# Optimization experiments

Measured on AMD Instinct MI355X. Metric: run time of the kernel, lower is better.

Reference implementation:

```python
import jax, jax.numpy as jnp
import numpy as np

N_HEADS = 64
HEAD_DIM = 128
ROPE_DIM = 64
TOPK = 2048
ROPE_BASE = 10000.0


def _rope(x, positions):
    # neox-style rotary on the first ROPE_DIM dims of the last axis
    half = ROPE_DIM // 2
    inv_freq = 1.0 / (ROPE_BASE ** (jnp.arange(half, dtype=jnp.float32) / half))
    ang = positions.astype(jnp.float32)[:, None] * inv_freq[None, :]  # [T, half]
    cos, sin = jnp.cos(ang), jnp.sin(ang)
    if x.ndim == 3:  # [T, H, D] -> broadcast over heads
        cos, sin = cos[:, None, :], sin[:, None, :]
    x1 = x[..., :half]
    x2 = x[..., half:ROPE_DIM]
    rest = x[..., ROPE_DIM:]
    return jnp.concatenate([x1 * cos - x2 * sin, x2 * cos + x1 * sin, rest], axis=-1)


def setup_inputs() -> dict:
    key = jax.random.key(0)
    ks = jax.random.split(key, 5)
    T, H_SIZE, QLR = 4096, 7168, 1536
    return {
        "hidden_states": jax.random.normal(ks[0], (T, H_SIZE), jnp.float32),
        "qr": jax.random.normal(ks[1], (T, QLR), jnp.float32),
        "positions": jnp.arange(T, dtype=jnp.int32),
        "wq_b": jax.random.normal(ks[2], (QLR, N_HEADS * HEAD_DIM), jnp.float32) * 0.02,
        "wk": jax.random.normal(ks[3], (H_SIZE, HEAD_DIM), jnp.float32) * 0.02,
        "k_gamma": jnp.ones((HEAD_DIM,), jnp.float32),
        "k_beta": jnp.zeros((HEAD_DIM,), jnp.float32),
        "w_proj": jax.random.normal(ks[4], (H_SIZE, N_HEADS), jnp.float32) * 0.02,
    }


def _index_scores(hidden_states, qr, positions, wq_b, wk, k_gamma, k_beta, w_proj):
    T = hidden_states.shape[0]
    # q projection from q_lora rank, per-head, RoPE on first ROPE_DIM dims, softmax scale
    q = (qr @ wq_b).reshape(T, N_HEADS, HEAD_DIM)
    q = _rope(q, positions) * (HEAD_DIM ** -0.5)
    # compressor: k projection + LayerNorm(eps=1e-6) + RoPE
    k = hidden_states @ wk  # [T, D]
    mu = jnp.mean(k, axis=-1, keepdims=True)
    var = jnp.mean((k - mu) ** 2, axis=-1, keepdims=True)
    k = (k - mu) * jax.lax.rsqrt(var + 1e-6) * k_gamma + k_beta
    k = _rope(k, positions)
    # per-head mixing weights, scaled by n_head**-0.5
    w = (hidden_states @ w_proj) * (N_HEADS ** -0.5)  # [T, H]

    # score[t, s] = sum_h w[t, h] * relu(q[t, h, :] . k[s, :])
    # accumulate over heads to avoid materializing [T, H, S]
    @jax.checkpoint
    def body(acc, hx):
        qh, wh = hx  # qh: [T, D], wh: [T]
        return acc + wh[:, None] * jax.nn.relu(qh @ k.T), None

    scores, _ = jax.lax.scan(
        body,
        jnp.zeros((T, T), jnp.float32),
        (jnp.transpose(q, (1, 0, 2)), w.T),
    )
    causal = positions[None, :] <= positions[:, None]
    return jnp.where(causal, scores, -jnp.inf)


def reference(hidden_states, qr, positions, wq_b, wk, k_gamma, k_beta, w_proj):
    scores = _index_scores(hidden_states, qr, positions, wq_b, wk, k_gamma, k_beta, w_proj)
    _, topk_idx = jax.lax.top_k(scores, TOPK)  # [T, TOPK] token indices for sparse attn
    return topk_idx, scores
```

## Files before the change

### kernel.cpp

```cpp
#include <hip/hip_runtime.h>
#include <hip/hip_bf16.h>
#include <math.h>

#define T_DIM 4096
#define HSZ   7168
#define QLR_K 1536
#define NH    64
#define HD    128
#define QN    (NH*HD)
#define TOPK_N 2048
#define MASK_VAL (-3.0e38f)
#define WSCALE 0.011048543456039806f

using short8 = __attribute__((ext_vector_type(8))) short;
using f32x4  = __attribute__((ext_vector_type(4))) float;
using i32x8  = __attribute__((ext_vector_type(8))) int;

#define MFMA16(a,b,c) __builtin_amdgcn_mfma_f32_16x16x32_bf16(a,b,c,0,0,0)
#define MFMA8(a,b,c)  __builtin_amdgcn_mfma_f32_16x16x32_fp8_fp8(a,b,c,0,0,0)
#define MFMA8S(a,b,c) __builtin_amdgcn_mfma_scale_f32_16x16x128_f8f6f4(a,b,c,0,0,0,127,0,127)

__device__ __forceinline__ float rope_invf(int d) {
    return (float)(1.0 / pow(10000.0, (double)d / 32.0));
}
__device__ __forceinline__ unsigned short f2bf(float f) {
    unsigned u = __float_as_uint(f);
    return (unsigned short)((u + 0x7FFFu + ((u >> 16) & 1u)) >> 16);
}
__device__ __forceinline__ unsigned char f2fp8(float x) {
    return (unsigned char)(__builtin_amdgcn_cvt_pk_fp8_f32(x, x, 0, false) & 0xFF);
}
__device__ __forceinline__ unsigned pk4fp8(float a, float b, float c, float d) {
    unsigned w = (unsigned)__builtin_amdgcn_cvt_pk_fp8_f32(a, b, 0, false);
    return (unsigned)__builtin_amdgcn_cvt_pk_fp8_f32(c, d, (int)w, true);
}

__global__ __launch_bounds__(256)
void rope_tab_kernel(const int* __restrict__ positions, float2* __restrict__ tab) {
    int idx = blockIdx.x * 256 + threadIdx.x;
    int t = idx >> 5, dd = idx & 31;
    float p = (float)positions[t];
    float ang = p * rope_invf(dd);
    float s, c; sincosf(ang, &s, &c);
    tab[idx] = make_float2(c, s);
}

__global__ __launch_bounds__(256)
void conv_afrag(const float* __restrict__ src, unsigned short* __restrict__ dst,
                int C, int KS, int ctiles) {
    __shared__ float lds[32][258];
    const int tid = threadIdx.x;
    const int rt = blockIdx.x / ctiles, ct = blockIdx.x - rt * ctiles;
    const int r0 = rt * 32, c0 = ct * 256;
#pragma unroll
    for (int it = 0; it < 8; ++it) {
        int fid = it * 256 + tid;
        int r = fid >> 6, c4 = (fid & 63) << 2;
        float4 v = *(const float4*)(src + (size_t)(r0 + r) * C + c0 + c4);
        lds[r][c4] = v.x; lds[r][c4 + 1] = v.y; lds[r][c4 + 2] = v.z; lds[r][c4 + 3] = v.w;
    }
    __syncthreads();
    const int lane = tid & 63, wid = tid >> 6;
#pragma unroll
    for (int j = 0; j < 4; ++j) {
        int s = wid * 4 + j;
        int ig_l = s >> 3, ks_l = s & 7;
        int r = ig_l * 16 + (lane & 15);
        int c = ks_l * 32 + ((lane >> 4) << 3);
        unsigned short o[8];
#pragma unroll
        for (int e = 0; e < 8; ++e) o[e] = f2bf(lds[r][c + e]);
        size_t ig = rt * 2 + ig_l, ks = (size_t)ct * 8 + ks_l;
        *(short8*)(dst + ((ig * KS + ks) * 64 + lane) * 8) = *(short8*)o;
    }
}

__global__ __launch_bounds__(256)
void conv_qr_fp8(const float* __restrict__ src, unsigned char* __restrict__ dst) {
    __shared__ float lds[32][258];
    const int tid = threadIdx.x;
    const int rt = blockIdx.x / 6, ct = blockIdx.x - rt * 6;
    const int r0 = rt * 32, c0 = ct * 256;
#pragma unroll
    for (int it = 0; it < 8; ++it) {
        int fid = it * 256 + tid;
        int r = fid >> 6, c4 = (fid & 63) << 2;
        float4 v = *(const float4*)(src + (size_t)(r0 + r) * QLR_K + c0 + c4);
        lds[r][c4] = v.x; lds[r][c4 + 1] = v.y; lds[r][c4 + 2] = v.z; lds[r][c4 + 3] = v.w;
    }
    __syncthreads();
    const int lane = tid & 63, wid = tid >> 6;
#pragma unroll
    for (int j = 0; j < 4; ++j) {
        int s = wid * 4 + j;
        int ig_l = s >> 3, ks_l = s & 7;
        int r = ig_l * 16 + (lane & 15);
        int c = ks_l * 32 + ((lane >> 4) << 3);
        uint2 o;
        o.x = pk4fp8(lds[r][c], lds[r][c + 1], lds[r][c + 2], lds[r][c + 3]);
        o.y = pk4fp8(lds[r][c + 4], lds[r][c + 5], lds[r][c + 6], lds[r][c + 7]);
        size_t ig = rt * 2 + ig_l;
        int ks = ct * 8 + ks_l;
        size_t off = ((ig * 12 + (ks >> 2)) * 64 + lane) * 32 + (ks & 3) * 8;
        *(uint2*)(dst + off) = o;
    }
}

__global__ __launch_bounds__(256)
void conv_wq_fp8(const float* __restrict__ wq, unsigned char* __restrict__ dst) {
    __shared__ float lds[32][258];
    const int tid = threadIdx.x;
    const int kt = blockIdx.x >> 5, nt = blockIdx.x & 31;
    const int k0 = kt * 32, n0 = nt * 256;
#pragma unroll
    for (int it = 0; it < 8; ++it) {
        int fid = it * 256 + tid;
        int k = fid >> 6, c4 = (fid & 63) << 2;
        float4 v = *(const float4*)(wq + (size_t)(k0 + k) * QN + n0 + c4);
        lds[k][c4] = v.x; lds[k][c4 + 1] = v.y; lds[k][c4 + 2] = v.z; lds[k][c4 + 3] = v.w;
    }
    __syncthreads();
    const int lane = tid & 63, wid = tid >> 6;
#pragma unroll
    for (int j = 0; j < 4; ++j) {
        int s = wid * 4 + j;
        int n_l = s * 16 + (lane & 15);
        int kb = (lane >> 4) << 3;
        uint2 o;
        o.x = pk4fp8(lds[kb][n_l], lds[kb + 1][n_l], lds[kb + 2][n_l], lds[kb + 3][n_l]);
        o.y = pk4fp8(lds[kb + 4][n_l], lds[kb + 5][n_l], lds[kb + 6][n_l], lds[kb + 7][n_l]);
        size_t ng = (size_t)nt * 16 + s;
        size_t off = ((ng * 12 + (kt >> 2)) * 64 + lane) * 32 + (kt & 3) * 8;
        *(uint2*)(dst + off) = o;
    }
}

__global__ __launch_bounds__(256)
void conv_wkw(const float* __restrict__ wk, const float* __restrict__ wp,
              unsigned short* __restrict__ dst) {
    int gid = blockIdx.x * 4 + (threadIdx.x >> 6);
    int lane = threadIdx.x & 63;
    int ng = gid / 224, ks = gid - ng * 224;
    int col = ng * 16 + (lane & 15);
    int k = ks * 32 + ((lane >> 4) << 3);
    unsigned short o[8];
#pragma unroll
    for (int e = 0; e < 8; ++e) {
        float v = (col < 128) ? wk[(size_t)(k + e) * 128 + col]
                              : wp[(size_t)(k + e) * 64 + (col - 128)];
        o[e] = f2bf(v);
    }
    *(short8*)(dst + ((size_t)gid * 64 + lane) * 8) = *(short8*)o;
}

__global__ __launch_bounds__(256, 4)
void kw_gemm_mfma(const unsigned short* __restrict__ hsfrag,
                  const unsigned short* __restrict__ wkwfrag,
                  float* __restrict__ part) {
    const int kz = blockIdx.x >> 8;
    const int ig = blockIdx.x & 255;
    const int lane = threadIdx.x & 63, wid = threadIdx.x >> 6;
    const f32x4 zed = {0.f, 0.f, 0.f, 0.f};
    f32x4 acc[3];
#pragma unroll
    for (int j = 0; j < 3; ++j) acc[j] = zed;

    const unsigned short* ap = hsfrag + ((size_t)ig * 224 * 64 + lane) * 8;
    const unsigned short* bp = wkwfrag + ((size_t)(wid * 3) * 224 * 64 + lane) * 8;
#pragma unroll 4
    for (int ks = kz * 56; ks < kz * 56 + 56; ++ks) {
        short8 a = *(const short8*)(ap + (size_t)ks * 512);
        short8 b0 = *(const short8*)(bp + (size_t)ks * 512);
        short8 b1 = *(const short8*)(bp + (size_t)(224 * 64 * 8) + (size_t)ks * 512);
        short8 b2 = *(const short8*)(bp + (size_t)(2 * 224 * 64 * 8) + (size_t)ks * 512);
        acc[0] = MFMA16(a, b0, acc[0]);
        acc[1] = MFMA16(a, b1, acc[1]);
        acc[2] = MFMA16(a, b2, acc[2]);
    }
    const int colc = lane & 15, rsub = (lane >> 4) << 2;
    float* pb = part + (size_t)kz * T_DIM * 192;
#pragma unroll
    for (int j = 0; j < 3; ++j) {
        int ng = wid * 3 + j;
#pragma unroll
        for (int r = 0; r < 4; ++r) {
            int row = ig * 16 + rsub + r;
            pb[(size_t)row * 192 + ng * 16 + colc] = acc[j][r];
        }
    }
}

__global__ __launch_bounds__(256)
void reduce_w(const float* __restrict__ part, float* __restrict__ wT) {
    __shared__ float lds[64][65];
    const int r0 = blockIdx.x * 64;
    const int tid = threadIdx.x;
#pragma unroll
    for (int it = 0; it < 16; ++it) {
        int fid = it * 256 + tid;
        int rl = fid >> 6, h = fid & 63;
        float s = 0.f;
#pragma unroll
        for (int z = 0; z < 4; ++z)
            s += part[((size_t)z * T_DIM + r0 + rl) * 192 + 128 + h];
        lds[rl][h] = s * WSCALE;
    }
    __syncthreads();
#pragma unroll
    for (int it = 0; it < 16; ++it) {
        int fid = it * 256 + tid;
        int h = fid >> 6, rl = fid & 63;
        wT[(size_t)h * T_DIM + r0 + rl] = lds[rl][h];
    }
}

__global__ __launch_bounds__(256)
void ln_rope_k(const float* __restrict__ part, const float2* __restrict__ tab,
               const float* __restrict__ gamma, const float* __restrict__ beta,
               unsigned char* __restrict__ kfrag) {
    __shared__ float ln[4][128];
    const int tid = threadIdx.x;
    const int wr = tid >> 6, lane = tid & 63;
    const int row = blockIdx.x * 4 + wr;
    float2 v = make_float2(0.f, 0.f);
#pragma unroll
    for (int z = 0; z < 4; ++z) {
        float2 p = *(const float2*)(part + ((size_t)z * T_DIM + row) * 192 + lane * 2);
        v.x += p.x; v.y += p.y;
    }
    float s = v.x + v.y;
#pragma unroll
    for (int off = 1; off < 64; off <<= 1) s += __shfl_xor(s, off);
    float mu = s * (1.0f / 128.0f);
    float d0 = v.x - mu, d1 = v.y - mu;
    float s2 = d0 * d0 + d1 * d1;
#pragma unroll
    for (int off = 1; off < 64; off <<= 1) s2 += __shfl_xor(s2, off);
    float rstd = 1.0f / sqrtf(s2 * (1.0f / 128.0f) + 1e-6f);
    ln[wr][lane * 2]     = d0 * rstd * gamma[lane * 2]     + beta[lane * 2];
    ln[wr][lane * 2 + 1] = d1 * rstd * gamma[lane * 2 + 1] + beta[lane * 2 + 1];
    __syncthreads();
    int d = lane * 2;
    float o0, o1;
    float v0 = ln[wr][d], v1 = ln[wr][d + 1];
    if (d < 64) {
        int dd = d & 31;
        float2 c0 = tab[(size_t)row * 32 + dd];
        float2 c1 = tab[(size_t)row * 32 + dd + 1];
        if (d < 32) {
            o0 = v0 * c0.x - ln[wr][d + 32] * c0.y;
            o1 = v1 * c1.x - ln[wr][d + 33] * c1.y;
        } else {
            o0 = v0 * c0.x + ln[wr][d - 32] * c0.y;
            o1 = v1 * c1.x + ln[wr][d - 31] * c1.y;
        }
    } else { o0 = v0; o1 = v1; }
    int jg = row >> 4, ks = d >> 5, sub = d & 31;
    int lp = ((sub >> 3) << 4) + (row & 15);
    size_t bidx = ((size_t)jg * 64 + lp) * 32 + ks * 8 + (sub & 7);
    unsigned pk = (unsigned)__builtin_amdgcn_cvt_pk_fp8_f32(o0, o1, 0, false);
    *(unsigned short*)(kfrag + bidx) = (unsigned short)(pk & 0xFFFFu);
}

__global__ __launch_bounds__(256, 2)
void q_gemm_mfma(const unsigned char* __restrict__ qr8,
                 const unsigned char* __restrict__ wq8,
                 const float2* __restrict__ tab,
                 unsigned char* __restrict__ qfrag) {
    const int hw = blockIdx.x;
    const int orig = (hw & 7) * 256 + (hw >> 3);
    const int head = orig >> 5, mt = orig & 31;
    const int tid = threadIdx.x, lane = tid & 63, wid = tid >> 6;
    const int wm = wid >> 1, wn = wid & 1;
    const f32x4 zed = {0.f, 0.f, 0.f, 0.f};
    f32x4 acc[4][4];
#pragma unroll
    for (int m = 0; m < 4; m++)
#pragma unroll
        for (int n = 0; n < 4; n++) acc[m][n] = zed;

    const int ig0 = mt * 8 + wm * 4;
    const int ng0 = head * 8 + wn * 4;
    const unsigned char* ap = qr8 + ((size_t)ig0 * 12 * 64 + lane) * 32;
    const unsigned char* bp = wq8 + ((size_t)ng0 * 12 * 64 + lane) * 32;
    for (int kq = 0; kq < 12; ++kq) {
        i32x8 a0_ = *(const i32x8*)(ap + (size_t)(0 * 12 + kq) * 2048);
        i32x8 a1_ = *(const i32x8*)(ap + (size_t)(1 * 12 + kq) * 2048);
        i32x8 a2_ = *(const i32x8*)(ap + (size_t)(2 * 12 + kq) * 2048);
        i32x8 a3_ = *(const i32x8*)(ap + (size_t)(3 * 12 + kq) * 2048);
#pragma unroll
        for (int n = 0; n < 4; n++) {
            i32x8 b = *(const i32x8*)(bp + ((size_t)n * 12 + kq) * 2048);
            acc[0][n] = MFMA8S(a0_, b, acc[0][n]);
            acc[1][n] = MFMA8S(a1_, b, acc[1][n]);
            acc[2][n] = MFMA8S(a2_, b, acc[2][n]);
            acc[3][n] = MFMA8S(a3_, b, acc[3][n]);
        }
    }
    const int colc = lane & 15;
    const int rsub = (lane >> 4) << 2;
#pragma unroll
    for (int m = 0; m < 4; m++) {
#pragma unroll
        for (int r = 0; r < 4; r++) {
            int row = mt * 128 + wm * 64 + m * 16 + rsub + r;
            int rl = rsub + r;
            size_t base = ((size_t)(row >> 4) * 64 + head) * 2048;
            if (wn == 0) {
#pragma unroll
                for (int n2 = 0; n2 < 2; n2++) {
                    int dd = n2 * 16 + colc;
                    float2 cs = tab[(size_t)row * 32 + dd];
                    float x1 = acc[m][n2][r], x2 = acc[m][n2 + 2][r];
                    float olo = x1 * cs.x - x2 * cs.y;
                    float ohi = x2 * cs.x + x1 * cs.y;
                    int lp = ((dd >> 3) << 4) + rl;
                    qfrag[base + lp * 32 + 0 * 8 + (dd & 7)] = f2fp8(olo);
                    qfrag[base + lp * 32 + 1 * 8 + (dd & 7)] = f2fp8(ohi);
                }
            } else {
#pragma unroll
                for (int n = 0; n < 4; n++) {
                    int d = 64 + n * 16 + colc;
                    int ks2 = d >> 5, sub = d & 31;
                    int lp = ((sub >> 3) << 4) + rl;
                    qfrag[base + lp * 32 + ks2 * 8 + (sub & 7)] = f2fp8(acc[m][n][r]);
                }
            }
        }
    }
}

#define SCOMP(A, hh) {                                                         \
    f32x4 s0 = MFMA8S(A, kf8[0], zed);                                         \
    f32x4 s1 = MFMA8S(A, kf8[1], zed);                                         \
    f32x4 s2 = MFMA8S(A, kf8[2], zed);                                         \
    f32x4 s3 = MFMA8S(A, kf8[3], zed);                                         \
    f32x4 s4 = MFMA8S(A, kf8[4], zed);                                         \
    f32x4 s5 = MFMA8S(A, kf8[5], zed);                                         \
    f32x4 s6 = MFMA8S(A, kf8[6], zed);                                         \
    f32x4 s7 = MFMA8S(A, kf8[7], zed);                                         \
    f32x4 wv = *(const f32x4*)&wlds[hh][wid * 16 + rsub];                      \
    _Pragma("unroll")                                                          \
    for (int rr_ = 0; rr_ < 4; ++rr_) {                                        \
        acc[0][rr_] += wv[rr_] * fmaxf(s0[rr_], 0.0f);                         \
        acc[1][rr_] += wv[rr_] * fmaxf(s1[rr_], 0.0f);                         \
        acc[2][rr_] += wv[rr_] * fmaxf(s2[rr_], 0.0f);                         \
        acc[3][rr_] += wv[rr_] * fmaxf(s3[rr_], 0.0f);                         \
        acc[4][rr_] += wv[rr_] * fmaxf(s4[rr_], 0.0f);                         \
        acc[5][rr_] += wv[rr_] * fmaxf(s5[rr_], 0.0f);                         \
        acc[6][rr_] += wv[rr_] * fmaxf(s6[rr_], 0.0f);                         \
        acc[7][rr_] += wv[rr_] * fmaxf(s7[rr_], 0.0f);                         \
    }                                                                          \
}

__global__ __launch_bounds__(256)
void scores_mfma(const unsigned char* __restrict__ qfrag,
                 const unsigned char* __restrict__ kfrag,
                 const float* __restrict__ wT, float* __restrict__ S) {
    const int bid = blockIdx.x;
    int u = (int)((sqrtf(4.f * bid + 1.f) - 1.f) * 0.5f);
    while ((u + 1) * (u + 2) <= bid) ++u;
    while (u * (u + 1) > bid) --u;
    int r_ = bid - u * (u + 1);
    const int byp = (r_ <= u) ? 2 * u : 2 * u + 1;
    const int jt  = (r_ <= u) ? r_ : r_ - (u + 1);
    __shared__ float wlds[64][64];
    const int tid = threadIdx.x;
    const int lane = tid & 63, wid = tid >> 6;
    const int i0 = byp * 64, j0 = jt * 128;
    const f32x4 zed = {0.f, 0.f, 0.f, 0.f};
#pragma unroll
    for (int it = 0; it < 16; ++it) {
        int fid = it * 256 + tid;
        int hh = fid >> 6, rl = fid & 63;
        wlds[hh][rl] = wT[(size_t)hh * T_DIM + i0 + rl];
    }
    i32x8 kf8[8];
#pragma unroll
    for (int n = 0; n < 8; ++n) {
        int jg = (j0 >> 4) + n;
        kf8[n] = *(const i32x8*)(kfrag + ((size_t)jg * 64 + lane) * 32);
    }
    __syncthreads();

    f32x4 acc[8];
#pragma unroll
    for (int n = 0; n < 8; n++) acc[n] = zed;

    const int rsub = (lane >> 4) << 2;
    const unsigned char* qb = qfrag + (size_t)(byp * 4 + wid) * 131072 + lane * 32;

    i32x8 a0 = *(const i32x8*)qb;
    for (int h = 0; h < NH; h += 2) {
        i32x8 a1 = *(const i32x8*)(qb + (size_t)(h + 1) * 2048);
        SCOMP(a0, h)
        if (h + 2 < NH) a0 = *(const i32x8*)(qb + (size_t)(h + 2) * 2048);
        SCOMP(a1, h + 1)
    }

    const int colc = lane & 15;
#pragma unroll
    for (int n = 0; n < 8; n++) {
        int col = j0 + n * 16 + colc;
#pragma unroll
        for (int rr = 0; rr < 4; rr++) {
            int row = i0 + wid * 16 + rsub + rr;
            float v = acc[n][rr];
            if (col > row) v = MASK_VAL;
            S[(size_t)row * T_DIM + col] = v;
        }
    }
}

__device__ __forceinline__ void ce(unsigned &x, unsigned &y, bool up) {
    unsigned lo = x < y ? x : y, hi = x < y ? y : x;
    x = up ? lo : hi; y = up ? hi : lo;
}
__device__ __forceinline__ unsigned cd(unsigned a, unsigned b, bool keep_lo) {
    unsigned lo = a < b ? a : b, hi = a < b ? b : a;
    return keep_lo ? lo : hi;
}

#define TK_SHFL(k, j) {                                                        \
    const bool kl_ = ((e0 & (k)) == 0u) ^ ((e0 & (j)) != 0u);                  \
    q0 = cd(q0, (unsigned)__shfl_xor((int)q0, (j) >> 2), kl_);                 \
    q1 = cd(q1, (unsigned)__shfl_xor((int)q1, (j) >> 2), kl_);                 \
    q2 = cd(q2, (unsigned)__shfl_xor((int)q2, (j) >> 2), kl_);                 \
    q3 = cd(q3, (unsigned)__shfl_xor((int)q3, (j) >> 2), kl_); }

#define TK_LDS(k, j) {                                                         \
    __syncthreads();                                                           \
    *(uint4*)&L[e0] = make_uint4(q0, q1, q2, q3);                              \
    __syncthreads();                                                           \
    uint4 p_ = *(uint4*)&L[e0 ^ (j)];                                          \
    const bool kl_ = ((e0 & (k)) == 0u) ^ ((e0 & (j)) != 0u);                  \
    q0 = cd(q0, p_.x, kl_); q1 = cd(q1, p_.y, kl_);                            \
    q2 = cd(q2, p_.z, kl_); q3 = cd(q3, p_.w, kl_); }

#define TK_REG(k) {                                                            \
    const bool up_ = ((e0 & (k)) == 0u);                                       \
    ce(q0, q2, up_); ce(q1, q3, up_);                                          \
    ce(q0, q1, up_); ce(q2, q3, up_); }

__global__ __launch_bounds__(1024)
void topk_kernel(const float* __restrict__ S, float* __restrict__ outIdx) {
    __shared__ unsigned lds[4096];
    const int bid = blockIdx.x;
    const int tid = threadIdx.x;

    unsigned q0, q1, q2, q3;
    int row; unsigned e0; unsigned* L;

    if (bid < 1024) {
        const int half = tid >> 9;
        row = bid * 2 + half;
        e0 = 4u * (tid & 511);
        L = &lds[half * 2048];
    } else {
        row = bid + 1024;
        e0 = 4u * tid;
        L = lds;
    }
    const unsigned N = (bid < 1024) ? 2048u : 4096u;

    {
        float4 f = *(const float4*)(S + (size_t)row * T_DIM + e0);
        const float* fp = &f.x;
        unsigned qq[4];
#pragma unroll
        for (int e = 0; e < 4; ++e) {
            unsigned p = e0 + e;
            unsigned u = __float_as_uint(fp[e]);
            u = (u & 0x80000000u) ? ~u : (u | 0x80000000u);
            unsigned key = ((~u) & 0xFFFFF000u) | p;
            qq[e] = ((int)p > row) ? (0xFFFFF000u | p) : key;
        }
        q0 = qq[0]; q1 = qq[1]; q2 = qq[2]; q3 = qq[3];
        ce(q0, q1, true); ce(q2, q3, false);
        bool up4 = (e0 & 4u) == 0;
        ce(q0, q2, up4); ce(q1, q3, up4);
        ce(q0, q1, up4); ce(q2, q3, up4);
    }

    TK_SHFL(8u, 4u)                                             TK_REG(8u)
    TK_SHFL(16u, 8u)  TK_SHFL(16u, 4u)                          TK_REG(16u)
    TK_SHFL(32u, 16u) TK_SHFL(32u, 8u)  TK_SHFL(32u, 4u)        TK_REG(32u)
    TK_SHFL(64u, 32u) TK_SHFL(64u, 16u) TK_SHFL(64u, 8u)
    TK_SHFL(64u, 4u)                                            TK_REG(64u)
    TK_SHFL(128u, 64u) TK_SHFL(128u, 32u) TK_SHFL(128u, 16u)
    TK_SHFL(128u, 8u)  TK_SHFL(128u, 4u)                        TK_REG(128u)
    TK_SHFL(256u, 128u) TK_SHFL(256u, 64u) TK_SHFL(256u, 32u)
    TK_SHFL(256u, 16u)  TK_SHFL(256u, 8u)  TK_SHFL(256u, 4u)    TK_REG(256u)
    TK_LDS(512u, 256u)
    TK_SHFL(512u, 128u) TK_SHFL(512u, 64u) TK_SHFL(512u, 32u)
    TK_SHFL(512u, 16u)  TK_SHFL(512u, 8u)  TK_SHFL(512u, 4u)    TK_REG(512u)
    TK_LDS(1024u, 512u) TK_LDS(1024u, 256u)
    TK_SHFL(1024u, 128u) TK_SHFL(1024u, 64u) TK_SHFL(1024u, 32u)
    TK_SHFL(1024u, 16u)  TK_SHFL(1024u, 8u)  TK_SHFL(1024u, 4u) TK_REG(1024u)
    TK_LDS(2048u, 1024u) TK_LDS(2048u, 512u) TK_LDS(2048u, 256u)
    TK_SHFL(2048u, 128u) TK_SHFL(2048u, 64u) TK_SHFL(2048u, 32u)
    TK_SHFL(2048u, 16u)  TK_SHFL(2048u, 8u)  TK_SHFL(2048u, 4u) TK_REG(2048u)

    if (N == 4096u) {
        __syncthreads();
        *(uint4*)&lds[e0] = make_uint4(q0, q1, q2, q3);
        __syncthreads();
        const bool low = e0 < 2048u;
        if (low) {
            uint4 p = *(uint4*)&lds[e0 + 2048];
            q0 = q0 < p.x ? q0 : p.x; q1 = q1 < p.y ? q1 : p.y;
            q2 = q2 < p.z ? q2 : p.z; q3 = q3 < p.w ? q3 : p.w;
        }
#define TK_MLDS(j) {                                                           \
        __syncthreads();                                                       \
        if (low) *(uint4*)&lds[e0] = make_uint4(q0, q1, q2, q3);               \
        __syncthreads();                                                       \
        if (low) {                                                             \
            uint4 p_ = *(uint4*)&lds[e0 ^ (j)];                                \
            const bool kl_ = (e0 & (j)) == 0u;                                 \
            q0 = cd(q0, p_.x, kl_); q1 = cd(q1, p_.y, kl_);                    \
            q2 = cd(q2, p_.z, kl_); q3 = cd(q3, p_.w, kl_); } }
#define TK_MSHFL(j) {                                                          \
        const bool kl_ = (e0 & (j)) == 0u;                                     \
        q0 = cd(q0, (unsigned)__shfl_xor((int)q0, (j) >> 2), kl_);             \
        q1 = cd(q1, (unsigned)__shfl_xor((int)q1, (j) >> 2), kl_);             \
        q2 = cd(q2, (unsigned)__shfl_xor((int)q2, (j) >> 2), kl_);             \
        q3 = cd(q3, (unsigned)__shfl_xor((int)q3, (j) >> 2), kl_); }
        TK_MLDS(1024u) TK_MLDS(512u) TK_MLDS(256u)
        if (low) {
            TK_MSHFL(128u) TK_MSHFL(64u) TK_MSHFL(32u)
            TK_MSHFL(16u)  TK_MSHFL(8u)  TK_MSHFL(4u)
            ce(q0, q2, true); ce(q1, q3, true);
            ce(q0, q1, true); ce(q2, q3, true);
            float4 o = make_float4((float)(q0 & 0xFFFu), (float)(q1 & 0xFFFu),
                                   (float)(q2 & 0xFFFu), (float)(q3 & 0xFFFu));
            *(float4*)(outIdx + (size_t)row * TOPK_N + e0) = o;
        }
    } else {
        float4 o = make_float4((float)(q0 & 0xFFFu), (float)(q1 & 0xFFFu),
                               (float)(q2 & 0xFFFu), (float)(q3 & 0xFFFu));
        *(float4*)(outIdx + (size_t)row * TOPK_N + e0) = o;
    }
}

extern "C" void kernel_launch(void* const* d_in, const int* in_sizes, int n_in,
                              void* d_out, int out_size, void* d_ws, size_t ws_size,
                              hipStream_t stream) {
    const float* hs      = (const float*)d_in[0];
    const float* qr      = (const float*)d_in[1];
    const int*   pos     = (const int*)  d_in[2];
    const float* wq_b    = (const float*)d_in[3];
    const float* wk      = (const float*)d_in[4];
    const float* k_gamma = (const float*)d_in[5];
    const float* k_beta  = (const float*)d_in[6];
    const float* w_proj  = (const float*)d_in[7];

    float* out     = (float*)d_out;
    float* out_idx = out;
    float* S       = out + (size_t)T_DIM * TOPK_N;

    char* wsp = (char*)d_ws;
    unsigned char*  qfrag  = (unsigned char*)wsp;  wsp += (size_t)67108864;
    unsigned short* hsfrag = (unsigned short*)qfrag;
    unsigned char*  qrfrag = (unsigned char*)wsp;  wsp += (size_t)12582912;
    unsigned char*  wqfrag = (unsigned char*)wsp;  wsp += (size_t)25165824;
    unsigned short* wkwfrag= (unsigned short*)wsp; wsp += (size_t)2752512;
    float*          part   = (float*)wsp;          wsp += (size_t)12582912;
    float*          wT     = (float*)wsp;          wsp += (size_t)1048576;
    unsigned char*  kfrag  = (unsigned char*)wsp;  wsp += (size_t)1048576;
    float2*         tab    = (float2*)wsp;         wsp += (size_t)1048576;

    rope_tab_kernel<<<512, 256, 0, stream>>>(pos, tab);
    conv_afrag <<<3584, 256, 0, stream>>>(hs, hsfrag, HSZ, 224, 28);
    conv_wkw   <<<672,  256, 0, stream>>>(wk, w_proj, wkwfrag);
    kw_gemm_mfma<<<1024, 256, 0, stream>>>(hsfrag, wkwfrag, part);
    reduce_w   <<<64,   256, 0, stream>>>(part, wT);
    ln_rope_k  <<<T_DIM / 4, 256, 0, stream>>>(part, tab, k_gamma, k_beta, kfrag);
    conv_qr_fp8<<<768,  256, 0, stream>>>(qr, qrfrag);
    conv_wq_fp8<<<1536, 256, 0, stream>>>(wq_b, wqfrag);
    q_gemm_mfma<<<2048, 256, 0, stream>>>(qrfrag, wqfrag, tab, qfrag);
    scores_mfma<<<1056, 256, 0, stream>>>(qfrag, kfrag, wT, S);
    topk_kernel<<<3072, 1024, 0, stream>>>(S, out_idx);
}
```

Baseline: 411.0 us.

## Process eight keys per thread in bitonic top-k, packing more rows per block

The bitonic top-k kernel now holds eight keys per thread instead of four. Each block sorts four short rows or two long rows instead of two short rows or one long row, which halves the grid. More of the sort network runs as in-register compare-exchanges, and fewer shuffle and LDS stages are needed per element, which cuts barrier and cross-lane traffic. The cost is higher register pressure and larger shared memory per block, which may lower occupancy.

```diff
diff --git a/kernel.cpp b/kernel.cpp
--- a/kernel.cpp
+++ b/kernel.cpp
@@ -422,54 +422,92 @@
     return keep_lo ? lo : hi;
 }
 
-#define TK_SHFL(k, j) {                                                        \
+#define CE8S(k, j) {                                                           \
     const bool kl_ = ((e0 & (k)) == 0u) ^ ((e0 & (j)) != 0u);                  \
-    q0 = cd(q0, (unsigned)__shfl_xor((int)q0, (j) >> 2), kl_);                 \
-    q1 = cd(q1, (unsigned)__shfl_xor((int)q1, (j) >> 2), kl_);                 \
-    q2 = cd(q2, (unsigned)__shfl_xor((int)q2, (j) >> 2), kl_);                 \
-    q3 = cd(q3, (unsigned)__shfl_xor((int)q3, (j) >> 2), kl_); }
-
-#define TK_LDS(k, j) {                                                         \
+    q0 = cd(q0, (unsigned)__shfl_xor((int)q0, (j) >> 3), kl_);                 \
+    q1 = cd(q1, (unsigned)__shfl_xor((int)q1, (j) >> 3), kl_);                 \
+    q2 = cd(q2, (unsigned)__shfl_xor((int)q2, (j) >> 3), kl_);                 \
+    q3 = cd(q3, (unsigned)__shfl_xor((int)q3, (j) >> 3), kl_);                 \
+    q4 = cd(q4, (unsigned)__shfl_xor((int)q4, (j) >> 3), kl_);                 \
+    q5 = cd(q5, (unsigned)__shfl_xor((int)q5, (j) >> 3), kl_);                 \
+    q6 = cd(q6, (unsigned)__shfl_xor((int)q6, (j) >> 3), kl_);                 \
+    q7 = cd(q7, (unsigned)__shfl_xor((int)q7, (j) >> 3), kl_); }
+
+#define CE8R(k) {                                                              \
+    const bool up_ = ((e0 & (k)) == 0u);                                       \
+    ce(q0, q4, up_); ce(q1, q5, up_); ce(q2, q6, up_); ce(q3, q7, up_);        \
+    ce(q0, q2, up_); ce(q1, q3, up_); ce(q4, q6, up_); ce(q5, q7, up_);        \
+    ce(q0, q1, up_); ce(q2, q3, up_); ce(q4, q5, up_); ce(q6, q7, up_); }
+
+#define CE8L(k, j) {                                                           \
     __syncthreads();                                                           \
-    *(uint4*)&L[e0] = make_uint4(q0, q1, q2, q3);                              \
+    *(uint4*)&L[e0]     = make_uint4(q0, q1, q2, q3);                          \
+    *(uint4*)&L[e0 + 4] = make_uint4(q4, q5, q6, q7);                          \
     __syncthreads();                                                           \
-    uint4 p_ = *(uint4*)&L[e0 ^ (j)];                                          \
+    uint4 pA_ = *(uint4*)&L[(e0 ^ (j))];                                       \
+    uint4 pB_ = *(uint4*)&L[(e0 ^ (j)) + 4];                                   \
     const bool kl_ = ((e0 & (k)) == 0u) ^ ((e0 & (j)) != 0u);                  \
-    q0 = cd(q0, p_.x, kl_); q1 = cd(q1, p_.y, kl_);                            \
-    q2 = cd(q2, p_.z, kl_); q3 = cd(q3, p_.w, kl_); }
-
-#define TK_REG(k) {                                                            \
-    const bool up_ = ((e0 & (k)) == 0u);                                       \
-    ce(q0, q2, up_); ce(q1, q3, up_);                                          \
-    ce(q0, q1, up_); ce(q2, q3, up_); }
+    q0 = cd(q0, pA_.x, kl_); q1 = cd(q1, pA_.y, kl_);                          \
+    q2 = cd(q2, pA_.z, kl_); q3 = cd(q3, pA_.w, kl_);                          \
+    q4 = cd(q4, pB_.x, kl_); q5 = cd(q5, pB_.y, kl_);                          \
+    q6 = cd(q6, pB_.z, kl_); q7 = cd(q7, pB_.w, kl_); }
+
+#define CM8L(j) {                                                              \
+    __syncthreads();                                                           \
+    if (low) {                                                                 \
+        *(uint4*)&L[e0]     = make_uint4(q0, q1, q2, q3);                      \
+        *(uint4*)&L[e0 + 4] = make_uint4(q4, q5, q6, q7);                      \
+    }                                                                          \
+    __syncthreads();                                                           \
+    if (low) {                                                                 \
+        uint4 pA_ = *(uint4*)&L[(e0 ^ (j))];                                   \
+        uint4 pB_ = *(uint4*)&L[(e0 ^ (j)) + 4];                               \
+        const bool kl_ = (e0 & (j)) == 0u;                                     \
+        q0 = cd(q0, pA_.x, kl_); q1 = cd(q1, pA_.y, kl_);                      \
+        q2 = cd(q2, pA_.z, kl_); q3 = cd(q3, pA_.w, kl_);                      \
+        q4 = cd(q4, pB_.x, kl_); q5 = cd(q5, pB_.y, kl_);                      \
+        q6 = cd(q6, pB_.z, kl_); q7 = cd(q7, pB_.w, kl_); } }
+
+#define CM8S(j) {                                                              \
+    const bool kl_ = (e0 & (j)) == 0u;                                         \
+    q0 = cd(q0, (unsigned)__shfl_xor((int)q0, (j) >> 3), kl_);                 \
+    q1 = cd(q1, (unsigned)__shfl_xor((int)q1, (j) >> 3), kl_);                 \
+    q2 = cd(q2, (unsigned)__shfl_xor((int)q2, (j) >> 3), kl_);                 \
+    q3 = cd(q3, (unsigned)__shfl_xor((int)q3, (j) >> 3), kl_);                 \
+    q4 = cd(q4, (unsigned)__shfl_xor((int)q4, (j) >> 3), kl_);                 \
+    q5 = cd(q5, (unsigned)__shfl_xor((int)q5, (j) >> 3), kl_);                 \
+    q6 = cd(q6, (unsigned)__shfl_xor((int)q6, (j) >> 3), kl_);                 \
+    q7 = cd(q7, (unsigned)__shfl_xor((int)q7, (j) >> 3), kl_); }
 
 __global__ __launch_bounds__(1024)
 void topk_kernel(const float* __restrict__ S, float* __restrict__ outIdx) {
-    __shared__ unsigned lds[4096];
+    __shared__ unsigned lds[8192];
     const int bid = blockIdx.x;
     const int tid = threadIdx.x;
 
-    unsigned q0, q1, q2, q3;
-    int row; unsigned e0; unsigned* L;
-
-    if (bid < 1024) {
-        const int half = tid >> 9;
-        row = bid * 2 + half;
-        e0 = 4u * (tid & 511);
-        L = &lds[half * 2048];
+    int row; unsigned e0; unsigned* L; bool longrow;
+    if (bid < 512) {
+        int slot = tid >> 8;
+        row = bid * 4 + slot;
+        e0 = 8u * (tid & 255);
+        L = &lds[slot * 2048];
+        longrow = false;
     } else {
-        row = bid + 1024;
-        e0 = 4u * tid;
-        L = lds;
-    }
-    const unsigned N = (bid < 1024) ? 2048u : 4096u;
-
+        int slot = tid >> 9;
+        row = 2048 + (bid - 512) * 2 + slot;
+        e0 = 8u * (tid & 511);
+        L = &lds[slot * 4096];
+        longrow = true;
+    }
+
+    unsigned q0, q1, q2, q3, q4, q5, q6, q7;
     {
-        float4 f = *(const float4*)(S + (size_t)row * T_DIM + e0);
-        const float* fp = &f.x;
-        unsigned qq[4];
-#pragma unroll
-        for (int e = 0; e < 4; ++e) {
+        float4 f0 = *(const float4*)(S + (size_t)row * T_DIM + e0);
+        float4 f1 = *(const float4*)(S + (size_t)row * T_DIM + e0 + 4);
+        const float fp[8] = {f0.x, f0.y, f0.z, f0.w, f1.x, f1.y, f1.z, f1.w};
+        unsigned qq[8];
+#pragma unroll
+        for (int e = 0; e < 8; ++e) {
             unsigned p = e0 + e;
             unsigned u = __float_as_uint(fp[e]);
             u = (u & 0x80000000u) ? ~u : (u | 0x80000000u);
@@ -477,70 +515,66 @@
             qq[e] = ((int)p > row) ? (0xFFFFF000u | p) : key;
         }
         q0 = qq[0]; q1 = qq[1]; q2 = qq[2]; q3 = qq[3];
-        ce(q0, q1, true); ce(q2, q3, false);
-        bool up4 = (e0 & 4u) == 0;
-        ce(q0, q2, up4); ce(q1, q3, up4);
-        ce(q0, q1, up4); ce(q2, q3, up4);
-    }
-
-    TK_SHFL(8u, 4u)                                             TK_REG(8u)
-    TK_SHFL(16u, 8u)  TK_SHFL(16u, 4u)                          TK_REG(16u)
-    TK_SHFL(32u, 16u) TK_SHFL(32u, 8u)  TK_SHFL(32u, 4u)        TK_REG(32u)
-    TK_SHFL(64u, 32u) TK_SHFL(64u, 16u) TK_SHFL(64u, 8u)
-    TK_SHFL(64u, 4u)                                            TK_REG(64u)
-    TK_SHFL(128u, 64u) TK_SHFL(128u, 32u) TK_SHFL(128u, 16u)
-    TK_SHFL(128u, 8u)  TK_SHFL(128u, 4u)                        TK_REG(128u)
-    TK_SHFL(256u, 128u) TK_SHFL(256u, 64u) TK_SHFL(256u, 32u)
-    TK_SHFL(256u, 16u)  TK_SHFL(256u, 8u)  TK_SHFL(256u, 4u)    TK_REG(256u)
-    TK_LDS(512u, 256u)
-    TK_SHFL(512u, 128u) TK_SHFL(512u, 64u) TK_SHFL(512u, 32u)
-    TK_SHFL(512u, 16u)  TK_SHFL(512u, 8u)  TK_SHFL(512u, 4u)    TK_REG(512u)
-    TK_LDS(1024u, 512u) TK_LDS(1024u, 256u)
-    TK_SHFL(1024u, 128u) TK_SHFL(1024u, 64u) TK_SHFL(1024u, 32u)
-    TK_SHFL(1024u, 16u)  TK_SHFL(1024u, 8u)  TK_SHFL(1024u, 4u) TK_REG(1024u)
-    TK_LDS(2048u, 1024u) TK_LDS(2048u, 512u) TK_LDS(2048u, 256u)
-    TK_SHFL(2048u, 128u) TK_SHFL(2048u, 64u) TK_SHFL(2048u, 32u)
-    TK_SHFL(2048u, 16u)  TK_SHFL(2048u, 8u)  TK_SHFL(2048u, 4u) TK_REG(2048u)
-
-    if (N == 4096u) {
+        q4 = qq[4]; q5 = qq[5]; q6 = qq[6]; q7 = qq[7];
+    }
+    ce(q0, q1, true);  ce(q2, q3, false); ce(q4, q5, true);  ce(q6, q7, false);
+    ce(q0, q2, true);  ce(q1, q3, true);  ce(q4, q6, false); ce(q5, q7, false);
+    ce(q0, q1, true);  ce(q2, q3, true);  ce(q4, q5, false); ce(q6, q7, false);
+    {
+        const bool up8 = ((e0 & 8u) == 0u);
+        ce(q0, q4, up8); ce(q1, q5, up8); ce(q2, q6, up8); ce(q3, q7, up8);
+        ce(q0, q2, up8); ce(q1, q3, up8); ce(q4, q6, up8); ce(q5, q7, up8);
+        ce(q0, q1, up8); ce(q2, q3, up8); ce(q4, q5, up8); ce(q6, q7, up8);
+    }
+    CE8S(16u, 8u)                                                CE8R(16u)
+    CE8S(32u, 16u)  CE8S(32u, 8u)                                CE8R(32u)
+    CE8S(64u, 32u)  CE8S(64u, 16u)  CE8S(64u, 8u)                CE8R(64u)
+    CE8S(128u, 64u) CE8S(128u, 32u) CE8S(128u, 16u) CE8S(128u, 8u) CE8R(128u)
+    CE8S(256u, 128u) CE8S(256u, 64u) CE8S(256u, 32u)
+    CE8S(256u, 16u)  CE8S(256u, 8u)                              CE8R(256u)
+    CE8S(512u, 256u) CE8S(512u, 128u) CE8S(512u, 64u)
+    CE8S(512u, 32u)  CE8S(512u, 16u)  CE8S(512u, 8u)             CE8R(512u)
+    CE8L(1024u, 512u)
+    CE8S(1024u, 256u) CE8S(1024u, 128u) CE8S(1024u, 64u)
+    CE8S(1024u, 32u)  CE8S(1024u, 16u)  CE8S(1024u, 8u)          CE8R(1024u)
+    CE8L(2048u, 1024u) CE8L(2048u, 512u)
+    CE8S(2048u, 256u) CE8S(2048u, 128u) CE8S(2048u, 64u)
+    CE8S(2048u, 32u)  CE8S(2048u, 16u)  CE8S(2048u, 8u)          CE8R(2048u)
+
+    if (!longrow) {
+        float4 o0 = make_float4((float)(q0 & 0xFFFu), (float)(q1 & 0xFFFu),
+                                (float)(q2 & 0xFFFu), (float)(q3 & 0xFFFu));
+        float4 o1 = make_float4((float)(q4 & 0xFFFu), (float)(q5 & 0xFFFu),
+                                (float)(q6 & 0xFFFu), (float)(q7 & 0xFFFu));
+        *(float4*)(outIdx + (size_t)row * TOPK_N + e0) = o0;
+        *(float4*)(outIdx + (size_t)row * TOPK_N + e0 + 4) = o1;
+    } else {
         __syncthreads();
-        *(uint4*)&lds[e0] = make_uint4(q0, q1, q2, q3);
+        *(uint4*)&L[e0]     = make_uint4(q0, q1, q2, q3);
+        *(uint4*)&L[e0 + 4] = make_uint4(q4, q5, q6, q7);
         __syncthreads();
         const bool low = e0 < 2048u;
         if (low) {
-            uint4 p = *(uint4*)&lds[e0 + 2048];
-            q0 = q0 < p.x ? q0 : p.x; q1 = q1 < p.y ? q1 : p.y;
-            q2 = q2 < p.z ? q2 : p.z; q3 = q3 < p.w ? q3 : p.w;
-        }
-#define TK_MLDS(j) {                                                           \
-        __syncthreads();                                                       \
-        if (low) *(uint4*)&lds[e0] = make_uint4(q0, q1, q2, q3);               \
-        __syncthreads();                                                       \
-        if (low) {                                                             \
-            uint4 p_ = *(uint4*)&lds[e0 ^ (j)];                                \
-            const bool kl_ = (e0 & (j)) == 0u;                                 \
-            q0 = cd(q0, p_.x, kl_); q1 = cd(q1, p_.y, kl_);                    \
-            q2 = cd(q2, p_.z, kl_); q3 = cd(q3, p_.w, kl_); } }
-#define TK_MSHFL(j) {                                                          \
-        const bool kl_ = (e0 & (j)) == 0u;                                     \
-        q0 = cd(q0, (unsigned)__shfl_xor((int)q0, (j) >> 2), kl_);             \
-        q1 = cd(q1, (unsigned)__shfl_xor((int)q1, (j) >> 2), kl_);             \
-        q2 = cd(q2, (unsigned)__shfl_xor((int)q2, (j) >> 2), kl_);             \
-        q3 = cd(q3, (unsigned)__shfl_xor((int)q3, (j) >> 2), kl_); }
-        TK_MLDS(1024u) TK_MLDS(512u) TK_MLDS(256u)
+            uint4 pA = *(uint4*)&L[e0 + 2048];
+            uint4 pB = *(uint4*)&L[e0 + 2048 + 4];
+            q0 = q0 < pA.x ? q0 : pA.x; q1 = q1 < pA.y ? q1 : pA.y;
+            q2 = q2 < pA.z ? q2 : pA.z; q3 = q3 < pA.w ? q3 : pA.w;
+            q4 = q4 < pB.x ? q4 : pB.x; q5 = q5 < pB.y ? q5 : pB.y;
+            q6 = q6 < pB.z ? q6 : pB.z; q7 = q7 < pB.w ? q7 : pB.w;
+        }
+        CM8L(1024u) CM8L(512u)
         if (low) {
-            TK_MSHFL(128u) TK_MSHFL(64u) TK_MSHFL(32u)
-            TK_MSHFL(16u)  TK_MSHFL(8u)  TK_MSHFL(4u)
-            ce(q0, q2, true); ce(q1, q3, true);
-            ce(q0, q1, true); ce(q2, q3, true);
-            float4 o = make_float4((float)(q0 & 0xFFFu), (float)(q1 & 0xFFFu),
-                                   (float)(q2 & 0xFFFu), (float)(q3 & 0xFFFu));
-            *(float4*)(outIdx + (size_t)row * TOPK_N + e0) = o;
-        }
-    } else {
-        float4 o = make_float4((float)(q0 & 0xFFFu), (float)(q1 & 0xFFFu),
-                               (float)(q2 & 0xFFFu), (float)(q3 & 0xFFFu));
-        *(float4*)(outIdx + (size_t)row * TOPK_N + e0) = o;
+            CM8S(256u) CM8S(128u) CM8S(64u) CM8S(32u) CM8S(16u) CM8S(8u)
+            ce(q0, q4, true); ce(q1, q5, true); ce(q2, q6, true); ce(q3, q7, true);
+            ce(q0, q2, true); ce(q1, q3, true); ce(q4, q6, true); ce(q5, q7, true);
+            ce(q0, q1, true); ce(q2, q3, true); ce(q4, q5, true); ce(q6, q7, true);
+            float4 o0 = make_float4((float)(q0 & 0xFFFu), (float)(q1 & 0xFFFu),
+                                    (float)(q2 & 0xFFFu), (float)(q3 & 0xFFFu));
+            float4 o1 = make_float4((float)(q4 & 0xFFFu), (float)(q5 & 0xFFFu),
+                                    (float)(q6 & 0xFFFu), (float)(q7 & 0xFFFu));
+            *(float4*)(outIdx + (size_t)row * TOPK_N + e0) = o0;
+            *(float4*)(outIdx + (size_t)row * TOPK_N + e0 + 4) = o1;
+        }
     }
 }
 
@@ -581,5 +615,5 @@
     conv_wq_fp8<<<1536, 256, 0, stream>>>(wq_b, wqfrag);
     q_gemm_mfma<<<2048, 256, 0, stream>>>(qrfrag, wqfrag, tab, qfrag);
     scores_mfma<<<1056, 256, 0, stream>>>(qfrag, kfrag, wT, S);
-    topk_kernel<<<3072, 1024, 0, stream>>>(S, out_idx);
-}
+    topk_kernel<<<1536, 1024, 0, stream>>>(S, out_idx);
+}
```

New measurement: 391.7 us, median of 2. 4.7% less time.
